# Kernel tuning notes

Measured on AMD Instinct MI355X. Metric: run time of the kernel, lower is better.

The kernel has to match this reference:

```python
import jax, jax.numpy as jnp
import numpy as np

TAU = 0.5

def setup_inputs() -> dict:
    key = jax.random.key(0)
    ks = jax.random.split(key, 6)
    B, L, D, P = 4, 4096, 256, 256
    return {
        "X1": jax.random.normal(ks[0], (B, L, D), dtype=jnp.float32),
        "X2": jax.random.normal(ks[1], (B, L, D), dtype=jnp.float32),
        "W1": jax.random.normal(ks[2], (P, D), dtype=jnp.float32) * (1.0 / np.sqrt(D)),
        "b1": jax.random.normal(ks[3], (P,), dtype=jnp.float32) * 0.01,
        "W2": jax.random.normal(ks[4], (D, P), dtype=jnp.float32) * (1.0 / np.sqrt(P)),
        "b2": jax.random.normal(ks[5], (D,), dtype=jnp.float32) * 0.01,
    }

def _projection(z, W1, b1, W2, b2):
    h = jax.nn.elu(z @ W1.T + b1)
    return h @ W2.T + b2

def _normalize(z, eps=1e-12):
    n = jnp.linalg.norm(z, axis=-1, keepdims=True)
    return z / jnp.maximum(n, eps)

def _semi_loss(z1, z2, tau):
    # z1, z2: [B, L, D]
    z1n = _normalize(z1)
    z2n = _normalize(z2)
    refl = jnp.exp(jnp.einsum('bld,bmd->blm', z1n, z1n) / tau)   # [B, L, L]
    between = jnp.exp(jnp.einsum('bld,bmd->blm', z1n, z2n) / tau)
    refl_diag = jnp.diagonal(refl, axis1=-2, axis2=-1)           # [B, L]
    between_diag = jnp.diagonal(between, axis1=-2, axis2=-1)
    denom = refl.sum(axis=-1) + between.sum(axis=-1) - refl_diag
    return -jnp.log(between_diag / denom).sum(axis=-1)           # [B]

def reference(X1, X2, W1, b1, W2, b2):
    h1 = _projection(X1, W1, b1, W2, b2)
    h2 = _projection(X2, W1, b1, W2, b2)
    l1 = _semi_loss(h1, h2, TAU)
    l2 = _semi_loss(h2, h1, TAU)
    return ((l1 + l2) * 0.5).mean()
```

## Files before the change

kernel.cpp:

```cpp
#include <hip/hip_runtime.h>
#include <math.h>


typedef __attribute__((ext_vector_type(8))) short short8;
typedef __attribute__((ext_vector_type(4))) short short4v;
typedef __attribute__((ext_vector_type(4))) float float4v;
typedef __attribute__((ext_vector_type(8))) int int8v;
typedef __attribute__((ext_vector_type(4))) int int4v;

__device__ __forceinline__ short f2bf(float f) {
    unsigned u = __builtin_bit_cast(unsigned, f);
    u += 0x7fffu + ((u >> 16) & 1u);
    return (short)(u >> 16);
}

__device__ __forceinline__ unsigned char f2fp8(float f) {
    float af = fabsf(f);
    unsigned s = (__builtin_bit_cast(unsigned, f) >> 31) << 7;
    if (af < 0.015625f) {
        int q = (int)rintf(af * 512.0f);
        return (unsigned char)(s | (unsigned)q);
    }
    unsigned au = __builtin_bit_cast(unsigned, af);
    au += 0x7FFFFu + ((au >> 20) & 1u);
    int e = (int)(au >> 23) - 127;
    unsigned m = (au >> 20) & 7u;
    return (unsigned char)(s | (unsigned)((e + 7) << 3) | m);
}

__device__ __forceinline__ void gl_lds16(const void* g, void* l) {
    __builtin_amdgcn_global_load_lds(
        (const __attribute__((address_space(1))) void*)g,
        (__attribute__((address_space(3))) void*)l, 16, 0, 0);
}

template <int RA, int RB, int NWM>
__device__ __forceinline__ void gemm512_core(
    const short* __restrict__ A, const short* __restrict__ B,
    int arow0, int brow0, short* lsA, short* lsB, float4v acc[4][4])
{
    const int tid  = threadIdx.x;
    const int w    = tid >> 6;
    const int lane = tid & 63;
    const int wm   = w % NWM;
    const int wn   = w / NWM;
    constexpr int ACH = RA / 8;

    for (int kt = 0; kt < 4; ++kt) {
        const int kbase = kt * 64;
#pragma unroll
        for (int r = 0; r < 6; ++r) {
            const int c = w * 6 + r;
            if (c < ACH) {
                const int s   = c * 64 + lane;
                const int kc  = s / RA;
                const int row = s % RA;
                gl_lds16(A + (size_t)(arow0 + row) * 256 + kbase + kc * 8,
                         lsA + (size_t)c * 512);
            } else {
                const int s   = (c - ACH) * 64 + lane;
                const int kc  = s / RB;
                const int row = s % RB;
                gl_lds16(B + (size_t)(brow0 + row) * 256 + kbase + kc * 8,
                         lsB + (size_t)(c - ACH) * 512);
            }
        }
        __syncthreads();
#pragma unroll
        for (int ks = 0; ks < 2; ++ks) {
            const int kc = ks * 4 + (lane >> 4);
            short8 af[4], bfv[4];
#pragma unroll
            for (int mi = 0; mi < 4; ++mi)
                af[mi] = *(const short8*)(lsA + ((size_t)kc * RA + wm * 64 + mi * 16 + (lane & 15)) * 8);
#pragma unroll
            for (int ni = 0; ni < 4; ++ni)
                bfv[ni] = *(const short8*)(lsB + ((size_t)kc * RB + wn * 64 + ni * 16 + (lane & 15)) * 8);
#pragma unroll
            for (int mi = 0; mi < 4; ++mi)
#pragma unroll
                for (int ni = 0; ni < 4; ++ni)
                    acc[mi][ni] = __builtin_amdgcn_mfma_f32_16x16x32_bf16(
                        af[mi], bfv[ni], acc[mi][ni], 0, 0, 0);
        }
        __syncthreads();
    }
}

__global__ __launch_bounds__(256) void convX_kernel(
    const float* __restrict__ X1, const float* __restrict__ X2,
    short* __restrict__ dst)
{
    int i = blockIdx.x * 256 + threadIdx.x;
    const float* src = (i < 1048576) ? X1 : X2;
    int j = i & 1048575;
    float4v v = ((const float4v*)src)[j];
    short4v o;
    o.x = f2bf(v.x); o.y = f2bf(v.y); o.z = f2bf(v.z); o.w = f2bf(v.w);
    ((short4v*)dst)[i] = o;
}

__global__ __launch_bounds__(256) void convW_kernel(
    const float* __restrict__ W1, const float* __restrict__ W2,
    short* __restrict__ d1, short* __restrict__ d2)
{
    int i = blockIdx.x * 256 + threadIdx.x;
    const float* src = (i < 16384) ? W1 : W2;
    short* dst = (i < 16384) ? d1 : d2;
    int j = i & 16383;
    float4v v = ((const float4v*)src)[j];
    short4v o;
    o.x = f2bf(v.x); o.y = f2bf(v.y); o.z = f2bf(v.z); o.w = f2bf(v.w);
    ((short4v*)dst)[j] = o;
}

__global__ __launch_bounds__(512) void proj1_kernel(
    const short* __restrict__ Xbf, const short* __restrict__ W1bf,
    const float* __restrict__ b1, short* __restrict__ Hbf)
{
    __shared__ short lsA[8192];
    __shared__ short lsB[16384];
    const int arow0 = blockIdx.x * 128;
    float4v acc[4][4];
#pragma unroll
    for (int mi = 0; mi < 4; ++mi)
#pragma unroll
        for (int ni = 0; ni < 4; ++ni)
            acc[mi][ni] = (float4v){0.f, 0.f, 0.f, 0.f};

    gemm512_core<128, 256, 2>(Xbf, W1bf, arow0, 0, lsA, lsB, acc);

    const int tid  = threadIdx.x;
    const int w    = tid >> 6;
    const int lane = tid & 63;
    const int wm   = w % 2;
    const int wn   = w / 2;
    const int rowbase = arow0 + wm * 64 + (lane >> 4) * 4;
    const int colbase = wn * 64 + (lane & 15);
#pragma unroll
    for (int ni = 0; ni < 4; ++ni) {
        const int col = colbase + ni * 16;
        const float bv = b1[col];
#pragma unroll
        for (int mi = 0; mi < 4; ++mi)
#pragma unroll
            for (int reg = 0; reg < 4; ++reg) {
                const int row = rowbase + mi * 16 + reg;
                float v = acc[mi][ni][reg] + bv;
                v = (v > 0.f) ? v : expm1f(v);
                Hbf[(size_t)row * 256 + col] = f2bf(v);
            }
    }
}

__global__ __launch_bounds__(512) void proj2norm_kernel(
    const short* __restrict__ Hbf, const short* __restrict__ W2bf,
    const float* __restrict__ b2, unsigned char* __restrict__ zn8)
{
    __shared__ short lsA[8192];
    __shared__ short lsB[16384];
    __shared__ float rssq[4][128];
    __shared__ float rinv[128];
    const int arow0 = blockIdx.x * 128;
    float4v acc[4][4];
#pragma unroll
    for (int mi = 0; mi < 4; ++mi)
#pragma unroll
        for (int ni = 0; ni < 4; ++ni)
            acc[mi][ni] = (float4v){0.f, 0.f, 0.f, 0.f};

    gemm512_core<128, 256, 2>(Hbf, W2bf, arow0, 0, lsA, lsB, acc);

    const int tid  = threadIdx.x;
    const int w    = tid >> 6;
    const int lane = tid & 63;
    const int wm   = w % 2;
    const int wn   = w / 2;

#pragma unroll
    for (int ni = 0; ni < 4; ++ni) {
        const float bv = b2[wn * 64 + ni * 16 + (lane & 15)];
#pragma unroll
        for (int mi = 0; mi < 4; ++mi)
#pragma unroll
            for (int reg = 0; reg < 4; ++reg)
                acc[mi][ni][reg] += bv;
    }
    float ps[4][4];
#pragma unroll
    for (int mi = 0; mi < 4; ++mi)
#pragma unroll
        for (int reg = 0; reg < 4; ++reg) {
            float s = 0.f;
#pragma unroll
            for (int ni = 0; ni < 4; ++ni) {
                float v = acc[mi][ni][reg];
                s += v * v;
            }
            s += __shfl_xor(s, 1); s += __shfl_xor(s, 2);
            s += __shfl_xor(s, 4); s += __shfl_xor(s, 8);
            ps[mi][reg] = s;
        }
    if ((lane & 15) == 0) {
        const int g = lane >> 4;
#pragma unroll
        for (int mi = 0; mi < 4; ++mi)
#pragma unroll
            for (int reg = 0; reg < 4; ++reg)
                rssq[wn][wm * 64 + mi * 16 + g * 4 + reg] = ps[mi][reg];
    }
    __syncthreads();
    if (tid < 128) {
        float ssq = rssq[0][tid] + rssq[1][tid] + rssq[2][tid] + rssq[3][tid];
        rinv[tid] = 1.41421356237f / fmaxf(sqrtf(ssq), 1e-12f);
    }
    __syncthreads();

    const int r0  = arow0;
    const int set = r0 >> 14;
    const int bb  = (r0 >> 12) & 3;
    const int l0  = r0 & 4095;
    unsigned char* dst = zn8 + ((size_t)(bb * 2 + set) * 4096 + l0) * 256;
    const int colbase = wn * 64 + (lane & 15);
#pragma unroll
    for (int mi = 0; mi < 4; ++mi)
#pragma unroll
        for (int reg = 0; reg < 4; ++reg) {
            const int rl = wm * 64 + mi * 16 + (lane >> 4) * 4 + reg;
            const float inv = rinv[rl];
#pragma unroll
            for (int ni = 0; ni < 4; ++ni)
                dst[(size_t)rl * 256 + colbase + ni * 16] =
                    f2fp8(acc[mi][ni][reg] * inv);
        }
}

#if defined(__has_builtin)
#if __has_builtin(__builtin_amdgcn_mfma_scale_f32_16x16x128_f8f6f4)
#define HAVE_MX 1
#endif
#endif

__global__ __launch_bounds__(512, 2) void gram_fp8_kernel(
    const unsigned char* __restrict__ zn8, float* __restrict__ S,
    float* __restrict__ out)
{
    __shared__ unsigned char lsB[2][32768];

    const int bx    = blockIdx.x;
    const int xcd   = bx & 7;
    const int batch = xcd >> 1;
    const int sub   = (bx >> 3) * 2 + (xcd & 1);
    const int stripe = sub >> 1;
    const int half   = sub & 1;
    const unsigned char* Z = zn8 + (size_t)batch * 2097152;
    const int q0 = stripe * 128;
    const int t0 = half * 32;
    const int djt = (q0 ^ 4096) >> 7;

    const int tid  = threadIdx.x;
    const int w    = tid >> 6;
    const int lane = tid & 63;
    const int wm   = w & 3;
    const int wn   = w >> 2;
    const int quad = lane >> 4;
    const int l15  = lane & 15;

#define STAGE_B(t, buf)                                                       \
    {                                                                         \
        const unsigned char* Bb = Z + (size_t)(t) * 128 * 256;                \
        _Pragma("unroll")                                                     \
        for (int r = 0; r < 4; ++r) {                                         \
            const int c   = w * 4 + r;                                        \
            const int u   = c * 64 + lane;                                    \
            const int kp  = u >> 7;                                           \
            const int col = u & 127;                                          \
            gl_lds16(Bb + (size_t)col * 256 + kp * 16,                        \
                     &lsB[buf][(size_t)c * 1024]);                            \
        }                                                                     \
    }

    float rs[2][4];
#pragma unroll
    for (int mi = 0; mi < 2; ++mi)
#pragma unroll
        for (int reg = 0; reg < 4; ++reg)
            rs[mi][reg] = 0.f;
    float dsum = 0.f;

#ifdef HAVE_MX
    int8v afr[2][2];
    {
        const unsigned char* Ab = Z + (size_t)(q0 + wm * 32) * 256;
#pragma unroll
        for (int mi = 0; mi < 2; ++mi)
#pragma unroll
            for (int ks = 0; ks < 2; ++ks) {
                const unsigned char* p = Ab + (size_t)(mi * 16 + l15) * 256
                                         + ks * 128 + quad * 32;
                int4v lo = *(const int4v*)p;
                int4v hi = *(const int4v*)(p + 16);
                afr[mi][ks] = __builtin_shufflevector(lo, hi, 0,1,2,3,4,5,6,7);
            }
    }

    STAGE_B(t0, 0);
    __syncthreads();

    for (int jt = 0; jt < 32; ++jt) {
        const int buf = jt & 1;
        if (jt < 31) STAGE_B(t0 + jt + 1, buf ^ 1);

        float4v acc[2][4];
#pragma unroll
        for (int mi = 0; mi < 2; ++mi)
#pragma unroll
            for (int ni = 0; ni < 4; ++ni)
                acc[mi][ni] = (float4v){0.f, 0.f, 0.f, 0.f};

        const unsigned char* lb = &lsB[buf][0];
#pragma unroll
        for (int ks = 0; ks < 2; ++ks) {
            const int kp0 = ks * 8 + quad * 2;
            int8v bfv[4];
#pragma unroll
            for (int ni = 0; ni < 4; ++ni) {
                const unsigned char* p = lb +
                    ((size_t)kp0 * 128 + wn * 64 + ni * 16 + l15) * 16;
                int4v lo = *(const int4v*)p;
                int4v hi = *(const int4v*)(p + 2048);
                bfv[ni] = __builtin_shufflevector(lo, hi, 0,1,2,3,4,5,6,7);
            }
#pragma unroll
            for (int mi = 0; mi < 2; ++mi)
#pragma unroll
                for (int ni = 0; ni < 4; ++ni)
                    acc[mi][ni] = __builtin_amdgcn_mfma_scale_f32_16x16x128_f8f6f4(
                        afr[mi][ks], bfv[ni], acc[mi][ni],
                        0, 0,
                        0, 0x7F7F7F7F,
                        0, 0x7F7F7F7F);
        }

        if (t0 + jt == djt) {
#pragma unroll
            for (int mi = 0; mi < 2; ++mi)
#pragma unroll
                for (int ni = 0; ni < 4; ++ni)
#pragma unroll
                    for (int reg = 0; reg < 4; ++reg) {
                        const int rg = q0 + wm * 32 + mi * 16 + quad * 4 + reg;
                        const int cg = djt * 128 + wn * 64 + ni * 16 + l15;
                        if ((rg ^ 4096) == cg) dsum += acc[mi][ni][reg];
                    }
        }

#pragma unroll
        for (int mi = 0; mi < 2; ++mi)
#pragma unroll
            for (int reg = 0; reg < 4; ++reg) {
                float s = 0.f;
#pragma unroll
                for (int ni = 0; ni < 4; ++ni)
                    s += __expf(acc[mi][ni][reg]);
                rs[mi][reg] += s;
            }

        __syncthreads();
    }
#else
    long afr[2][8];
    {
        const unsigned char* Ab = Z + (size_t)(q0 + wm * 32) * 256;
#pragma unroll
        for (int mi = 0; mi < 2; ++mi)
#pragma unroll
            for (int kc = 0; kc < 8; ++kc)
                afr[mi][kc] = *(const long*)(Ab + (size_t)(mi * 16 + l15) * 256
                                             + kc * 32 + quad * 8);
    }
    STAGE_B(t0, 0);
    __syncthreads();
    for (int jt = 0; jt < 32; ++jt) {
        const int buf = jt & 1;
        if (jt < 31) STAGE_B(t0 + jt + 1, buf ^ 1);
        float4v acc[2][4];
#pragma unroll
        for (int mi = 0; mi < 2; ++mi)
#pragma unroll
            for (int ni = 0; ni < 4; ++ni)
                acc[mi][ni] = (float4v){0.f, 0.f, 0.f, 0.f};
        const unsigned char* lb = &lsB[buf][0];
#pragma unroll
        for (int kc = 0; kc < 8; ++kc) {
            const int kseg = kc * 4 + quad;
            const int kp   = kseg >> 1;
            const int hf   = kseg & 1;
            long bfv[4];
#pragma unroll
            for (int ni = 0; ni < 4; ++ni)
                bfv[ni] = *(const long*)(lb +
                    ((size_t)kp * 128 + wn * 64 + ni * 16 + l15) * 16 + hf * 8);
#pragma unroll
            for (int mi = 0; mi < 2; ++mi)
#pragma unroll
                for (int ni = 0; ni < 4; ++ni)
                    acc[mi][ni] = __builtin_amdgcn_mfma_f32_16x16x32_fp8_fp8(
                        afr[mi][kc], bfv[ni], acc[mi][ni], 0, 0, 0);
        }
        if (t0 + jt == djt) {
#pragma unroll
            for (int mi = 0; mi < 2; ++mi)
#pragma unroll
                for (int ni = 0; ni < 4; ++ni)
#pragma unroll
                    for (int reg = 0; reg < 4; ++reg) {
                        const int rg = q0 + wm * 32 + mi * 16 + quad * 4 + reg;
                        const int cg = djt * 128 + wn * 64 + ni * 16 + l15;
                        if ((rg ^ 4096) == cg) dsum += acc[mi][ni][reg];
                    }
        }
#pragma unroll
        for (int mi = 0; mi < 2; ++mi)
#pragma unroll
            for (int reg = 0; reg < 4; ++reg) {
                float s = 0.f;
#pragma unroll
                for (int ni = 0; ni < 4; ++ni)
                    s += __expf(acc[mi][ni][reg]);
                rs[mi][reg] += s;
            }
        __syncthreads();
    }
#endif

#pragma unroll
    for (int mi = 0; mi < 2; ++mi)
#pragma unroll
        for (int reg = 0; reg < 4; ++reg) {
            float v = rs[mi][reg];
            v += __shfl_xor(v, 1); v += __shfl_xor(v, 2);
            v += __shfl_xor(v, 4); v += __shfl_xor(v, 8);
            rs[mi][reg] = v;
        }
    if (l15 == 0) {
        float* Sq = S + (size_t)batch * 8192 + q0 + wm * 32;
#pragma unroll
        for (int mi = 0; mi < 2; ++mi)
#pragma unroll
            for (int reg = 0; reg < 4; ++reg)
                atomicAdd(&Sq[mi * 16 + quad * 4 + reg], rs[mi][reg]);
    }
    {
        float dv = dsum;
        dv += __shfl_xor(dv, 1);  dv += __shfl_xor(dv, 2);
        dv += __shfl_xor(dv, 4);  dv += __shfl_xor(dv, 8);
        dv += __shfl_xor(dv, 16); dv += __shfl_xor(dv, 32);
        if (lane == 0 && dv != 0.f)
            atomicAdd(out, -0.125f * dv);
    }
#undef STAGE_B
}

__global__ __launch_bounds__(256) void final_log_kernel(
    const float* __restrict__ S, float* __restrict__ out)
{
    __shared__ float red[4];
    const int tid  = threadIdx.x;
    const int w    = tid >> 6;
    const int lane = tid & 63;
    const float E2 = 7.3890560989306495f;
    float acc = 0.f;
    for (int i = blockIdx.x * 256 + tid; i < 32768; i += gridDim.x * 256)
        acc += logf(S[i] - E2);
    acc += __shfl_xor(acc, 1);  acc += __shfl_xor(acc, 2);
    acc += __shfl_xor(acc, 4);  acc += __shfl_xor(acc, 8);
    acc += __shfl_xor(acc, 16); acc += __shfl_xor(acc, 32);
    if (lane == 0) red[w] = acc;
    __syncthreads();
    if (tid == 0)
        atomicAdd(out, 0.125f * (red[0] + red[1] + red[2] + red[3]));
}

extern "C" void kernel_launch(void* const* d_in, const int* in_sizes, int n_in,
                              void* d_out, int out_size, void* d_ws, size_t ws_size,
                              hipStream_t stream)
{
    const float* X1 = (const float*)d_in[0];
    const float* X2 = (const float*)d_in[1];
    const float* W1 = (const float*)d_in[2];
    const float* b1 = (const float*)d_in[3];
    const float* W2 = (const float*)d_in[4];
    const float* b2 = (const float*)d_in[5];

    char* ws = (char*)d_ws;
    float* S    = (float*)(ws + 0);
    short* W1bf = (short*)(ws + 131072);
    short* W2bf = (short*)(ws + 262144);
    short* Xbf  = (short*)(ws + 393216);
    unsigned char* zn8 = (unsigned char*)(ws + 393216);
    short* Hbf  = (short*)(ws + 17170432);

    hipMemsetAsync(S, 0, 131072, stream);
    hipMemsetAsync(d_out, 0, sizeof(float), stream);

    convW_kernel<<<128, 256, 0, stream>>>(W1, W2, W1bf, W2bf);
    convX_kernel<<<8192, 256, 0, stream>>>(X1, X2, Xbf);
    proj1_kernel<<<256, 512, 0, stream>>>(Xbf, W1bf, b1, Hbf);
    proj2norm_kernel<<<256, 512, 0, stream>>>(Hbf, W2bf, b2, zn8);
    gram_fp8_kernel<<<512, 512, 0, stream>>>(zn8, S, (float*)d_out);
    final_log_kernel<<<64, 256, 0, stream>>>(S, (float*)d_out);
}
```

Measured before the change: 242.3 us.

## Use 256-thread blocks with larger per-wave tiles in projection and gram kernels

Projection GEMMs now run 64-row tiles per 256-thread block, with each of four waves owning 64 output columns, and twice as many blocks. The gram kernel also drops to 4 waves, each computing a 64x64 tile (4x4 MFMA accumulators), so each staged B tile is reused across more rows per wave. The aim is more blocks per CU for the projections and more MFMA work per LDS B read in the gram kernel. The cost is higher register pressure and fewer waves per block to hide latency, and W1/W2 are staged twice as often in the projections.

```diff
diff --git a/kernel.cpp b/kernel.cpp
--- a/kernel.cpp
+++ b/kernel.cpp
@@ -34,35 +34,32 @@
         (__attribute__((address_space(3))) void*)l, 16, 0, 0);
 }
 
-template <int RA, int RB, int NWM>
-__device__ __forceinline__ void gemm512_core(
+__device__ __forceinline__ void gemm256_core(
     const short* __restrict__ A, const short* __restrict__ B,
-    int arow0, int brow0, short* lsA, short* lsB, float4v acc[4][4])
+    int arow0, short* lsA, short* lsB, float4v acc[4][4])
 {
     const int tid  = threadIdx.x;
     const int w    = tid >> 6;
     const int lane = tid & 63;
-    const int wm   = w % NWM;
-    const int wn   = w / NWM;
-    constexpr int ACH = RA / 8;
+    const int l15  = lane & 15;
 
     for (int kt = 0; kt < 4; ++kt) {
         const int kbase = kt * 64;
 #pragma unroll
-        for (int r = 0; r < 6; ++r) {
-            const int c = w * 6 + r;
-            if (c < ACH) {
+        for (int r = 0; r < 10; ++r) {
+            const int c = w * 10 + r;
+            if (c < 8) {
                 const int s   = c * 64 + lane;
-                const int kc  = s / RA;
-                const int row = s % RA;
+                const int kc  = s >> 6;
+                const int row = s & 63;
                 gl_lds16(A + (size_t)(arow0 + row) * 256 + kbase + kc * 8,
                          lsA + (size_t)c * 512);
             } else {
-                const int s   = (c - ACH) * 64 + lane;
-                const int kc  = s / RB;
-                const int row = s % RB;
-                gl_lds16(B + (size_t)(brow0 + row) * 256 + kbase + kc * 8,
-                         lsB + (size_t)(c - ACH) * 512);
+                const int s   = (c - 8) * 64 + lane;
+                const int kc  = s >> 8;
+                const int row = s & 255;
+                gl_lds16(B + (size_t)row * 256 + kbase + kc * 8,
+                         lsB + (size_t)(c - 8) * 512);
             }
         }
         __syncthreads();
@@ -72,10 +69,10 @@
             short8 af[4], bfv[4];
 #pragma unroll
             for (int mi = 0; mi < 4; ++mi)
-                af[mi] = *(const short8*)(lsA + ((size_t)kc * RA + wm * 64 + mi * 16 + (lane & 15)) * 8);
+                af[mi] = *(const short8*)(lsA + ((size_t)kc * 64 + mi * 16 + l15) * 8);
 #pragma unroll
             for (int ni = 0; ni < 4; ++ni)
-                bfv[ni] = *(const short8*)(lsB + ((size_t)kc * RB + wn * 64 + ni * 16 + (lane & 15)) * 8);
+                bfv[ni] = *(const short8*)(lsB + ((size_t)kc * 256 + w * 64 + ni * 16 + l15) * 8);
 #pragma unroll
             for (int mi = 0; mi < 4; ++mi)
 #pragma unroll
@@ -114,13 +111,13 @@
     ((short4v*)dst)[j] = o;
 }
 
-__global__ __launch_bounds__(512) void proj1_kernel(
+__global__ __launch_bounds__(256, 4) void proj1_kernel(
     const short* __restrict__ Xbf, const short* __restrict__ W1bf,
     const float* __restrict__ b1, short* __restrict__ Hbf)
 {
-    __shared__ short lsA[8192];
+    __shared__ short lsA[4096];
     __shared__ short lsB[16384];
-    const int arow0 = blockIdx.x * 128;
+    const int arow0 = blockIdx.x * 64;
     float4v acc[4][4];
 #pragma unroll
     for (int mi = 0; mi < 4; ++mi)
@@ -128,15 +125,13 @@
         for (int ni = 0; ni < 4; ++ni)
             acc[mi][ni] = (float4v){0.f, 0.f, 0.f, 0.f};
 
-    gemm512_core<128, 256, 2>(Xbf, W1bf, arow0, 0, lsA, lsB, acc);
+    gemm256_core(Xbf, W1bf, arow0, lsA, lsB, acc);
 
     const int tid  = threadIdx.x;
     const int w    = tid >> 6;
     const int lane = tid & 63;
-    const int wm   = w % 2;
-    const int wn   = w / 2;
-    const int rowbase = arow0 + wm * 64 + (lane >> 4) * 4;
-    const int colbase = wn * 64 + (lane & 15);
+    const int rowbase = arow0 + (lane >> 4) * 4;
+    const int colbase = w * 64 + (lane & 15);
 #pragma unroll
     for (int ni = 0; ni < 4; ++ni) {
         const int col = colbase + ni * 16;
@@ -153,15 +148,15 @@
     }
 }
 
-__global__ __launch_bounds__(512) void proj2norm_kernel(
+__global__ __launch_bounds__(256, 4) void proj2norm_kernel(
     const short* __restrict__ Hbf, const short* __restrict__ W2bf,
     const float* __restrict__ b2, unsigned char* __restrict__ zn8)
 {
-    __shared__ short lsA[8192];
+    __shared__ short lsA[4096];
     __shared__ short lsB[16384];
-    __shared__ float rssq[4][128];
-    __shared__ float rinv[128];
-    const int arow0 = blockIdx.x * 128;
+    __shared__ float rssq[4][64];
+    __shared__ float rinv[64];
+    const int arow0 = blockIdx.x * 64;
     float4v acc[4][4];
 #pragma unroll
     for (int mi = 0; mi < 4; ++mi)
@@ -169,17 +164,17 @@
         for (int ni = 0; ni < 4; ++ni)
             acc[mi][ni] = (float4v){0.f, 0.f, 0.f, 0.f};
 
-    gemm512_core<128, 256, 2>(Hbf, W2bf, arow0, 0, lsA, lsB, acc);
+    gemm256_core(Hbf, W2bf, arow0, lsA, lsB, acc);
 
     const int tid  = threadIdx.x;
     const int w    = tid >> 6;
     const int lane = tid & 63;
-    const int wm   = w % 2;
-    const int wn   = w / 2;
+    const int quad = lane >> 4;
+    const int l15  = lane & 15;
 
 #pragma unroll
     for (int ni = 0; ni < 4; ++ni) {
-        const float bv = b2[wn * 64 + ni * 16 + (lane & 15)];
+        const float bv = b2[w * 64 + ni * 16 + l15];
 #pragma unroll
         for (int mi = 0; mi < 4; ++mi)
 #pragma unroll
@@ -201,16 +196,15 @@
             s += __shfl_xor(s, 4); s += __shfl_xor(s, 8);
             ps[mi][reg] = s;
         }
-    if ((lane & 15) == 0) {
-        const int g = lane >> 4;
+    if (l15 == 0) {
 #pragma unroll
         for (int mi = 0; mi < 4; ++mi)
 #pragma unroll
             for (int reg = 0; reg < 4; ++reg)
-                rssq[wn][wm * 64 + mi * 16 + g * 4 + reg] = ps[mi][reg];
+                rssq[w][mi * 16 + quad * 4 + reg] = ps[mi][reg];
     }
     __syncthreads();
-    if (tid < 128) {
+    if (tid < 64) {
         float ssq = rssq[0][tid] + rssq[1][tid] + rssq[2][tid] + rssq[3][tid];
         rinv[tid] = 1.41421356237f / fmaxf(sqrtf(ssq), 1e-12f);
     }
@@ -221,12 +215,12 @@
     const int bb  = (r0 >> 12) & 3;
     const int l0  = r0 & 4095;
     unsigned char* dst = zn8 + ((size_t)(bb * 2 + set) * 4096 + l0) * 256;
-    const int colbase = wn * 64 + (lane & 15);
+    const int colbase = w * 64 + l15;
 #pragma unroll
     for (int mi = 0; mi < 4; ++mi)
 #pragma unroll
         for (int reg = 0; reg < 4; ++reg) {
-            const int rl = wm * 64 + mi * 16 + (lane >> 4) * 4 + reg;
+            const int rl = mi * 16 + quad * 4 + reg;
             const float inv = rinv[rl];
 #pragma unroll
             for (int ni = 0; ni < 4; ++ni)
@@ -241,7 +235,7 @@
 #endif
 #endif
 
-__global__ __launch_bounds__(512, 2) void gram_fp8_kernel(
+__global__ __launch_bounds__(256, 2) void gram_fp8_kernel(
     const unsigned char* __restrict__ zn8, float* __restrict__ S,
     float* __restrict__ out)
 {
@@ -261,8 +255,8 @@
     const int tid  = threadIdx.x;
     const int w    = tid >> 6;
     const int lane = tid & 63;
-    const int wm   = w & 3;
-    const int wn   = w >> 2;
+    const int wm   = w & 1;
+    const int wn   = w >> 1;
     const int quad = lane >> 4;
     const int l15  = lane & 15;
 
@@ -270,8 +264,8 @@
     {                                                                         \
         const unsigned char* Bb = Z + (size_t)(t) * 128 * 256;                \
         _Pragma("unroll")                                                     \
-        for (int r = 0; r < 4; ++r) {                                         \
-            const int c   = w * 4 + r;                                        \
+        for (int r = 0; r < 8; ++r) {                                         \
+            const int c   = w * 8 + r;                                        \
             const int u   = c * 64 + lane;                                    \
             const int kp  = u >> 7;                                           \
             const int col = u & 127;                                          \
@@ -280,20 +274,20 @@
         }                                                                     \
     }
 
-    float rs[2][4];
-#pragma unroll
-    for (int mi = 0; mi < 2; ++mi)
+    float rs[4][4];
+#pragma unroll
+    for (int mi = 0; mi < 4; ++mi)
 #pragma unroll
         for (int reg = 0; reg < 4; ++reg)
             rs[mi][reg] = 0.f;
     float dsum = 0.f;
 
 #ifdef HAVE_MX
-    int8v afr[2][2];
+    int8v afr[4][2];
     {
-        const unsigned char* Ab = Z + (size_t)(q0 + wm * 32) * 256;
-#pragma unroll
-        for (int mi = 0; mi < 2; ++mi)
+        const unsigned char* Ab = Z + (size_t)(q0 + wm * 64) * 256;
+#pragma unroll
+        for (int mi = 0; mi < 4; ++mi)
 #pragma unroll
             for (int ks = 0; ks < 2; ++ks) {
                 const unsigned char* p = Ab + (size_t)(mi * 16 + l15) * 256
@@ -311,9 +305,9 @@
         const int buf = jt & 1;
         if (jt < 31) STAGE_B(t0 + jt + 1, buf ^ 1);
 
-        float4v acc[2][4];
-#pragma unroll
-        for (int mi = 0; mi < 2; ++mi)
+        float4v acc[4][4];
+#pragma unroll
+        for (int mi = 0; mi < 4; ++mi)
 #pragma unroll
             for (int ni = 0; ni < 4; ++ni)
                 acc[mi][ni] = (float4v){0.f, 0.f, 0.f, 0.f};
@@ -332,7 +326,7 @@
                 bfv[ni] = __builtin_shufflevector(lo, hi, 0,1,2,3,4,5,6,7);
             }
 #pragma unroll
-            for (int mi = 0; mi < 2; ++mi)
+            for (int mi = 0; mi < 4; ++mi)
 #pragma unroll
                 for (int ni = 0; ni < 4; ++ni)
                     acc[mi][ni] = __builtin_amdgcn_mfma_scale_f32_16x16x128_f8f6f4(
@@ -344,19 +338,19 @@
 
         if (t0 + jt == djt) {
 #pragma unroll
-            for (int mi = 0; mi < 2; ++mi)
+            for (int mi = 0; mi < 4; ++mi)
 #pragma unroll
                 for (int ni = 0; ni < 4; ++ni)
 #pragma unroll
                     for (int reg = 0; reg < 4; ++reg) {
-                        const int rg = q0 + wm * 32 + mi * 16 + quad * 4 + reg;
+                        const int rg = q0 + wm * 64 + mi * 16 + quad * 4 + reg;
                         const int cg = djt * 128 + wn * 64 + ni * 16 + l15;
                         if ((rg ^ 4096) == cg) dsum += acc[mi][ni][reg];
                     }
         }
 
 #pragma unroll
-        for (int mi = 0; mi < 2; ++mi)
+        for (int mi = 0; mi < 4; ++mi)
 #pragma unroll
             for (int reg = 0; reg < 4; ++reg) {
                 float s = 0.f;
@@ -369,11 +363,11 @@
         __syncthreads();
     }
 #else
-    long afr[2][8];
+    long afr[4][8];
     {
-        const unsigned char* Ab = Z + (size_t)(q0 + wm * 32) * 256;
-#pragma unroll
-        for (int mi = 0; mi < 2; ++mi)
+        const unsigned char* Ab = Z + (size_t)(q0 + wm * 64) * 256;
+#pragma unroll
+        for (int mi = 0; mi < 4; ++mi)
 #pragma unroll
             for (int kc = 0; kc < 8; ++kc)
                 afr[mi][kc] = *(const long*)(Ab + (size_t)(mi * 16 + l15) * 256
@@ -384,9 +378,9 @@
     for (int jt = 0; jt < 32; ++jt) {
         const int buf = jt & 1;
         if (jt < 31) STAGE_B(t0 + jt + 1, buf ^ 1);
-        float4v acc[2][4];
-#pragma unroll
-        for (int mi = 0; mi < 2; ++mi)
+        float4v acc[4][4];
+#pragma unroll
+        for (int mi = 0; mi < 4; ++mi)
 #pragma unroll
             for (int ni = 0; ni < 4; ++ni)
                 acc[mi][ni] = (float4v){0.f, 0.f, 0.f, 0.f};
@@ -402,7 +396,7 @@
                 bfv[ni] = *(const long*)(lb +
                     ((size_t)kp * 128 + wn * 64 + ni * 16 + l15) * 16 + hf * 8);
 #pragma unroll
-            for (int mi = 0; mi < 2; ++mi)
+            for (int mi = 0; mi < 4; ++mi)
 #pragma unroll
                 for (int ni = 0; ni < 4; ++ni)
                     acc[mi][ni] = __builtin_amdgcn_mfma_f32_16x16x32_fp8_fp8(
@@ -410,18 +404,18 @@
         }
         if (t0 + jt == djt) {
 #pragma unroll
-            for (int mi = 0; mi < 2; ++mi)
+            for (int mi = 0; mi < 4; ++mi)
 #pragma unroll
                 for (int ni = 0; ni < 4; ++ni)
 #pragma unroll
                     for (int reg = 0; reg < 4; ++reg) {
-                        const int rg = q0 + wm * 32 + mi * 16 + quad * 4 + reg;
+                        const int rg = q0 + wm * 64 + mi * 16 + quad * 4 + reg;
                         const int cg = djt * 128 + wn * 64 + ni * 16 + l15;
                         if ((rg ^ 4096) == cg) dsum += acc[mi][ni][reg];
                     }
         }
 #pragma unroll
-        for (int mi = 0; mi < 2; ++mi)
+        for (int mi = 0; mi < 4; ++mi)
 #pragma unroll
             for (int reg = 0; reg < 4; ++reg) {
                 float s = 0.f;
@@ -435,7 +429,7 @@
 #endif
 
 #pragma unroll
-    for (int mi = 0; mi < 2; ++mi)
+    for (int mi = 0; mi < 4; ++mi)
 #pragma unroll
         for (int reg = 0; reg < 4; ++reg) {
             float v = rs[mi][reg];
@@ -444,9 +438,9 @@
             rs[mi][reg] = v;
         }
     if (l15 == 0) {
-        float* Sq = S + (size_t)batch * 8192 + q0 + wm * 32;
-#pragma unroll
-        for (int mi = 0; mi < 2; ++mi)
+        float* Sq = S + (size_t)batch * 8192 + q0 + wm * 64;
+#pragma unroll
+        for (int mi = 0; mi < 4; ++mi)
 #pragma unroll
             for (int reg = 0; reg < 4; ++reg)
                 atomicAdd(&Sq[mi * 16 + quad * 4 + reg], rs[mi][reg]);
@@ -506,8 +500,8 @@
 
     convW_kernel<<<128, 256, 0, stream>>>(W1, W2, W1bf, W2bf);
     convX_kernel<<<8192, 256, 0, stream>>>(X1, X2, Xbf);
-    proj1_kernel<<<256, 512, 0, stream>>>(Xbf, W1bf, b1, Hbf);
-    proj2norm_kernel<<<256, 512, 0, stream>>>(Hbf, W2bf, b2, zn8);
-    gram_fp8_kernel<<<512, 512, 0, stream>>>(zn8, S, (float*)d_out);
+    proj1_kernel<<<512, 256, 0, stream>>>(Xbf, W1bf, b1, Hbf);
+    proj2norm_kernel<<<512, 256, 0, stream>>>(Hbf, W2bf, b2, zn8);
+    gram_fp8_kernel<<<512, 256, 0, stream>>>(zn8, S, (float*)d_out);
     final_log_kernel<<<64, 256, 0, stream>>>(S, (float*)d_out);
 }
```

New measurement: 217.8 us. 10.1% less time.
